# Optimization experiments

Hardware: AMD Instinct MI355X
Metric: run time of the kernel (lower is better)

## Reference

```python
import jax, jax.numpy as jnp
import numpy as np

D = 2048  # input_dimensions (== seq_len, required by the module's math)
H = 8192  # hidden_dimensions
B = 4
S = D


def setup_inputs() -> dict:
    key = jax.random.key(0)
    ks = jax.random.split(key, 13)
    scale_in = 1.0 / np.sqrt(D)
    scale_hid = 1.0 / np.sqrt(H)
    def lin(k, fan_in, fan_out, s):
        return jax.random.normal(k, (fan_in, fan_out), jnp.float32) * s
    inp = {"x": jax.random.normal(ks[0], (B, S, D), jnp.float32)}
    names = ["q", "k", "v"]
    for i, n in enumerate(names):
        inp[f"{n}_w1"] = lin(ks[1 + 4 * i], D, H, scale_in)
        inp[f"{n}_b1"] = jnp.zeros((H,), jnp.float32)
        inp[f"{n}_w2"] = lin(ks[2 + 4 * i], H, D, scale_hid)
        inp[f"{n}_b2"] = jnp.zeros((D,), jnp.float32)
    return inp


def _mlp(x, w1, b1, w2, b2):
    # Linear(D,H) -> ReLU -> Linear(H,D)
    h = jax.nn.relu(jnp.einsum("bsd,dh->bsh", x, w1) + b1)
    return jnp.einsum("bsh,hd->bsd", h, w2) + b2


def reference(x, q_w1, q_b1, q_w2, q_b2, k_w1, k_b1, k_w2, k_b2,
              v_w1, v_b1, v_w2, v_b2):
    Q = _mlp(x, q_w1, q_b1, q_w2, q_b2)
    K = _mlp(x, k_w1, k_b1, k_w2, k_b2)
    V = _mlp(x, v_w1, v_b1, v_w2, v_b2)
    # scores: Q @ K^T  -> [B, S, S]  (no 1/sqrt(d) scaling in original)
    scores = jnp.einsum("bsd,btd->bst", Q, K)
    # nn.Softmax(dim=1): over axis 1 (rows), NOT the usual last axis
    probs = jax.nn.softmax(scores, axis=1)
    # original computes V @ probs (requires S == D)
    out = jnp.einsum("bsd,bdt->bst", V, probs)
    return out
```

## Files before the change

### kernel.cpp

```cpp
#include <hip/hip_runtime.h>
#include <cstdint>
#include <cstddef>

typedef __attribute__((ext_vector_type(8))) short short8;
typedef __attribute__((ext_vector_type(4))) short short4v;
typedef __attribute__((ext_vector_type(4))) float f32x4;
typedef __attribute__((ext_vector_type(4))) int i32x4;

#define DEV __device__ __forceinline__

constexpr int DD = 2048;
constexpr int HHID = 8192;
constexpr int BB = 4;
constexpr int SS = 2048;
constexpr size_t NX = (size_t)BB * SS * DD;
constexpr size_t NW = (size_t)DD * HHID;
constexpr size_t NH = (size_t)BB * SS * HHID;

constexpr size_t OFF_XH  = 0;
constexpr size_t OFF_XA1 = OFF_XH + NX * 2;
constexpr size_t OFF_XA2 = OFF_XA1 + NX;
constexpr size_t OFF_WA1 = OFF_XA2 + NX;
constexpr size_t OFF_WA2 = OFF_WA1 + NW;
constexpr size_t OFF_WHV = OFF_WA1;
constexpr size_t OFF_HH  = OFF_WA2 + NW;
constexpr size_t OFF_HL  = OFF_HH + NH * 2;
constexpr size_t OFF_QKH = OFF_HL + NH * 2;
constexpr size_t OFF_QKL = OFF_QKH + NX * 2;
constexpr size_t OFF_QA1 = OFF_QKL + NX * 2;
constexpr size_t OFF_QA2 = OFF_QA1 + NX;
constexpr size_t OFF_KA1 = OFF_QA2 + NX;
constexpr size_t OFF_KA2 = OFF_KA1 + NX;
constexpr size_t OFF_HA1 = OFF_KA2 + NX;
constexpr size_t OFF_HA2 = OFF_HA1 + NH;
constexpr size_t OFF_V   = OFF_HA2 + NH;
constexpr size_t OFF_XS  = OFF_V + NX * 2;
constexpr size_t OFF_HS  = OFF_XS + 32768;
constexpr size_t OFF_QS  = OFF_HS + 32768;
constexpr size_t OFF_KS  = OFF_QS + 32768;
constexpr size_t OFF_CM  = OFF_KS + 32768;
constexpr size_t WS_TOTAL = OFF_CM + 32768;
constexpr size_t OFF_ST = OFF_HH;
constexpr size_t OFF_PT = OFF_HL;

__device__ __align__(256) unsigned char g_ws[WS_TOTAL];

DEV unsigned char* wsbase(unsigned char* p) { return p ? p : (unsigned char*)g_ws; }
DEV short f2bf(float v) { __bf16 b = (__bf16)v; return __builtin_bit_cast(short, b); }
DEV float bf2f(short s) { return (float)__builtin_bit_cast(__bf16, s); }

template <typename T> DEV void nts(T v, T* p) { __builtin_nontemporal_store(v, p); }
template <typename T> DEV T ntl(const T* p) { return __builtin_nontemporal_load(p); }

DEV void gl16(const short* g, short* l) {
  __builtin_amdgcn_global_load_lds((const __attribute__((address_space(1))) void*)g,
                                   (__attribute__((address_space(3))) void*)l, 16, 0, 0);
}
DEV void gl16b(const signed char* g, signed char* l) {
  __builtin_amdgcn_global_load_lds((const __attribute__((address_space(1))) void*)g,
                                   (__attribute__((address_space(3))) void*)l, 16, 0, 0);
}

DEV void raster2d(int rem, int gx, int grp, int& by, int& bx) {
  const int tpg = grp * gx;
  const int gidx = rem / tpg;
  const int o = rem - gidx * tpg;
  const int r = o / grp;
  by = gidx * grp + (o - r * grp);
  bx = r;
}

__global__ void cast_hi_k(const float* __restrict__ x, unsigned char* wsb,
                          size_t oh, size_t n4) {
  unsigned char* ws = wsbase(wsb);
  short4v* OH = (short4v*)(ws + oh);
  const f32x4* X = (const f32x4*)x;
  for (size_t i = (size_t)blockIdx.x * blockDim.x + threadIdx.x; i < n4;
       i += (size_t)gridDim.x * blockDim.x) {
    const f32x4 v = ntl(&X[i]);
    short4v hs;
#pragma unroll
    for (int e = 0; e < 4; ++e) hs[e] = f2bf(v[e]);
    OH[i] = hs;
  }
}

__launch_bounds__(256)
__global__ void quant_x_k(const float* __restrict__ x, unsigned char* wsb,
                          size_t oa1, size_t oa2, size_t oxs) {
  unsigned char* ws = wsbase(wsb);
  signed char* A1 = (signed char*)(ws + oa1);
  signed char* A2 = (signed char*)(ws + oa2);
  float* XS = (float*)(ws + oxs);
  const int row = blockIdx.x;
  const float* xr = x + (size_t)row * 2048;
  const int tid = threadIdx.x, lane = tid & 63;
  const f32x4 v0 = *(const f32x4*)&xr[tid * 8];
  const f32x4 v1 = *(const f32x4*)&xr[tid * 8 + 4];
  float m = 0.0f;
#pragma unroll
  for (int e = 0; e < 4; ++e) m = fmaxf(m, fmaxf(fabsf(v0[e]), fabsf(v1[e])));
#pragma unroll
  for (int o = 32; o; o >>= 1) m = fmaxf(m, __shfl_xor(m, o));
  __shared__ float rb[4];
  if (lane == 0) rb[tid >> 6] = m;
  __syncthreads();
  m = fmaxf(fmaxf(rb[0], rb[1]), fmaxf(rb[2], rb[3]));
  const float inv = (m > 1e-30f) ? 127.0f / m : 0.0f;
  if (tid == 0) XS[row] = m * (1.0f / 127.0f);
  unsigned int w1a = 0, w1b = 0, w2a = 0, w2b = 0;
#pragma unroll
  for (int e = 0; e < 8; ++e) {
    const float xv = (e < 4) ? v0[e] : v1[e - 4];
    const float q = xv * inv;
    const float a1f = rintf(q);
    int ia2 = (int)rintf((q - a1f) * 256.0f);
    ia2 = ia2 > 127 ? 127 : (ia2 < -127 ? -127 : ia2);
    const unsigned int b1 = (unsigned char)(signed char)(int)a1f;
    const unsigned int b2 = (unsigned char)(signed char)ia2;
    if (e < 4) { w1a |= b1 << (8 * e); w2a |= b2 << (8 * e); }
    else       { w1b |= b1 << (8 * (e - 4)); w2b |= b2 << (8 * (e - 4)); }
  }
  const size_t o = (size_t)row * 2048 + tid * 8;
  *(unsigned int*)&A1[o] = w1a; *(unsigned int*)&A1[o + 4] = w1b;
  *(unsigned int*)&A2[o] = w2a; *(unsigned int*)&A2[o + 4] = w2b;
}

__launch_bounds__(1024)
__global__ void rowquant_k(unsigned char* wsb, size_t hho, size_t hlo,
                           size_t oa1, size_t oa2, size_t oso, int rowlen) {
  unsigned char* ws = wsbase(wsb);
  const int row = blockIdx.x, tid = threadIdx.x, lane = tid & 63, wv = tid >> 6;
  const int nw = blockDim.x >> 6;
  const short8 hi = ntl((const short8*)((const short*)(ws + hho) + (size_t)row * rowlen) + tid);
  const short8 lo = ntl((const short8*)((const short*)(ws + hlo) + (size_t)row * rowlen) + tid);
  float v[8]; float m = 0.0f;
#pragma unroll
  for (int e = 0; e < 8; ++e) {
    v[e] = bf2f(hi[e]) + bf2f(lo[e]);
    m = fmaxf(m, fabsf(v[e]));
  }
#pragma unroll
  for (int o = 32; o; o >>= 1) m = fmaxf(m, __shfl_xor(m, o));
  __shared__ float rb[16];
  if (lane == 0) rb[wv] = m;
  __syncthreads();
  m = rb[0];
  for (int i = 1; i < nw; ++i) m = fmaxf(m, rb[i]);
  const float inv = (m > 1e-30f) ? 127.0f / m : 0.0f;
  if (tid == 0) ((float*)(ws + oso))[row] = m * (1.0f / 127.0f);
  unsigned int w1a = 0, w1b = 0, w2a = 0, w2b = 0;
#pragma unroll
  for (int e = 0; e < 8; ++e) {
    const float q = v[e] * inv;
    const float a1f = rintf(q);
    int ia2 = (int)rintf((q - a1f) * 256.0f);
    ia2 = ia2 > 127 ? 127 : (ia2 < -127 ? -127 : ia2);
    const unsigned int b1 = (unsigned char)(signed char)(int)a1f;
    const unsigned int b2 = (unsigned char)(signed char)ia2;
    if (e < 4) { w1a |= b1 << (8 * e); w2a |= b2 << (8 * e); }
    else       { w1b |= b1 << (8 * (e - 4)); w2b |= b2 << (8 * (e - 4)); }
  }
  const size_t o = (size_t)row * rowlen + tid * 8;
  signed char* A1 = (signed char*)(ws + oa1);
  signed char* A2 = (signed char*)(ws + oa2);
  *(unsigned int*)&A1[o] = w1a; *(unsigned int*)&A1[o + 4] = w1b;
  *(unsigned int*)&A2[o] = w2a; *(unsigned int*)&A2[o + 4] = w2b;
}

__launch_bounds__(256)
__global__ void colmax_k(const float* __restrict__ w, unsigned char* wsb,
                         size_t omax, int R, int C) {
  unsigned char* ws = wsbase(wsb);
  unsigned int* MX = (unsigned int*)(ws + omax);
  const int col = blockIdx.x * 256 + threadIdx.x;
  const int r0 = blockIdx.y * 128;
  float m = 0.0f;
  for (int r = 0; r < 128; ++r) m = fmaxf(m, fabsf(w[(size_t)(r0 + r) * C + col]));
  atomicMax(&MX[col], __float_as_uint(m));
}

__global__ void scalefix_k(unsigned char* wsb, size_t off, int n) {
  unsigned char* ws = wsbase(wsb);
  const int i = blockIdx.x * 256 + threadIdx.x;
  if (i < n) {
    float* p = (float*)(ws + off);
    const unsigned int u = ((const unsigned int*)p)[i];
    p[i] = __uint_as_float(u) * (1.0f / 127.0f);
  }
}

__global__ void transpose_quant_k(const float* __restrict__ src, unsigned char* wsb,
                                  size_t oa1, size_t oa2, size_t osc, int R, int C) {
  __shared__ float t[32][33];
  unsigned char* ws = wsbase(wsb);
  signed char* A1 = (signed char*)(ws + oa1);
  signed char* A2 = (signed char*)(ws + oa2);
  const float* SC = (const float*)(ws + osc);
  const int c0 = blockIdx.x << 5, r0 = blockIdx.y << 5;
  const int x = threadIdx.x, y = threadIdx.y;
#pragma unroll
  for (int i = 0; i < 4; ++i) {
    const int rr = y + (i << 3);
    t[rr][x] = ntl(&src[(size_t)(r0 + rr) * C + c0 + x]);
  }
  __syncthreads();
#pragma unroll
  for (int i = 0; i < 4; ++i) {
    const int oc = y + (i << 3);
    const float v = t[x][oc];
    const float s = SC[c0 + oc];
    const float inv = (s > 1e-38f) ? 1.0f / s : 0.0f;
    const float q = v * inv;
    const float a1f = rintf(q);
    int ia2 = (int)rintf((q - a1f) * 256.0f);
    ia2 = ia2 > 127 ? 127 : (ia2 < -127 ? -127 : ia2);
    const size_t o = (size_t)(c0 + oc) * R + r0 + x;
    A1[o] = (signed char)(int)a1f;
    A2[o] = (signed char)ia2;
  }
}

__global__ void transpose_cast_k(const float* __restrict__ src, unsigned char* wsb,
                                 size_t oh, int R, int C) {
  __shared__ float t[32][33];
  unsigned char* ws = wsbase(wsb);
  short* OH = (short*)(ws + oh);
  const int c0 = blockIdx.x << 5, r0 = blockIdx.y << 5;
  const int x = threadIdx.x, y = threadIdx.y;
#pragma unroll
  for (int i = 0; i < 4; ++i) {
    const int rr = y + (i << 3);
    t[rr][x] = ntl(&src[(size_t)(r0 + rr) * C + c0 + x]);
  }
  __syncthreads();
#pragma unroll
  for (int i = 0; i < 4; ++i) {
    const int oc = y + (i << 3);
    OH[(size_t)(c0 + oc) * R + r0 + x] = f2bf(t[x][oc]);
  }
}

DEV i32x4 mfma_i8(i32x4 a, i32x4 b, i32x4 c) {
  return __builtin_amdgcn_mfma_i32_16x16x64_i8(a, b, c, 0, 0, 0);
}
DEV i32x4 rfi8(const signed char* base, int lstride, int L, int row, int fg) {
  return *(const i32x4*)&base[L * lstride + row * 64 + ((fg ^ ((row >> 1) & 3)) << 4)];
}

template <bool RELU, int STORE>
__launch_bounds__(512, 2)
__global__ void gemm_i8_k(unsigned char* wsb,
                          size_t a1o, size_t a2o, size_t b1o, size_t b2o,
                          size_t aso, size_t bso, const float* __restrict__ bias,
                          size_t o0, size_t o1, int M, int N, int K,
                          int gx, int gxy, int grp) {
  __shared__ alignas(16) signed char lds8[114688];

  unsigned char* ws = wsbase(wsb);
  const int tid = threadIdx.x;
  const int lane = tid & 63;
  const int wave = tid >> 6;
  const int wm = (wave >> 2) << 6;
  const int wn = (wave & 3) << 6;
  const int fr = lane & 15;
  const int fg = lane >> 4;

  const int nwg = gridDim.x;
  const int q8 = nwg >> 3;
  const int id = (blockIdx.x & 7) * q8 + (blockIdx.x >> 3);
  const int bz = id / gxy;
  const int rem = id - bz * gxy;
  int by, bx;
  raster2d(rem, gx, grp, by, bx);
  const int brow = by << 7;
  const int bcol = bx << 8;

  const size_t batchA = (size_t)bz * M * K;
  const size_t batchB = (STORE == 2) ? (size_t)bz * N * K : 0;
  const signed char* Xa1 = (const signed char*)(ws + a1o) + batchA;
  const signed char* Xa2 = (const signed char*)(ws + a2o) + batchA;
  const signed char* Wa1 = (const signed char*)(ws + b1o) + batchB;
  const signed char* Wa2 = (const signed char*)(ws + b2o) + batchB;
  const float* AS = (const float*)(ws + aso) + (size_t)bz * M;
  const float* BS = (const float*)(ws + bso) + ((STORE == 2) ? (size_t)bz * N : 0);

  const int ar = tid >> 2, ac = tid & 3;
  const size_t aOff = (size_t)(brow + ar) * K + ((ac ^ ((ar >> 1) & 3)) << 4);
  size_t bOff[2];
#pragma unroll
  for (int h = 0; h < 2; ++h) {
    const int G = tid + h * 512;
    const int r = G >> 2, c = G & 3;
    bOff[h] = (size_t)(bcol + r) * K + ((c ^ ((r >> 1) & 3)) << 4);
  }

  auto stageA = [&](int slotBase, int tt) {
    const int ko = tt * 64;
    gl16b(Xa1 + aOff + ko, &lds8[slotBase + (tid << 4)]);
    gl16b(Xa2 + aOff + ko, &lds8[slotBase + 8192 + (tid << 4)]);
  };
  auto stageB = [&](int slotBase, int tt) {
    const int ko = tt * 64;
#pragma unroll
    for (int h = 0; h < 2; ++h) {
      gl16b(Wa1 + bOff[h] + ko, &lds8[slotBase + ((tid + h * 512) << 4)]);
      gl16b(Wa2 + bOff[h] + ko, &lds8[slotBase + 16384 + ((tid + h * 512) << 4)]);
    }
  };

  const int nt = K / 64;
  i32x4 I1[4][4] = {};
  i32x4 I2[4][4] = {};

  stageA(0, 0);
  stageB(49152, 0);
  if (nt > 1) { stageA(16384, 1); stageB(49152 + 32768, 1); }
  if (nt > 1) { asm volatile("s_waitcnt vmcnt(6)" ::: "memory"); }
  else        { asm volatile("s_waitcnt vmcnt(0)" ::: "memory"); }
  __builtin_amdgcn_s_barrier();

  for (int t = 0; t < nt; ++t) {
    const signed char* aS = &lds8[(t % 3) * 16384];
    const signed char* bS = &lds8[49152 + (t & 1) * 32768];
    const int sA2 = ((t + 2) % 3) * 16384;
    const int sB2 = 49152 + (t & 1) * 32768;
    const bool pf = (t + 2 < nt);
    i32x4 bf[4][2], af[2][2];

    if (pf) stageA(sA2, t + 2);
#pragma unroll
    for (int j = 0; j < 4; ++j) {
      bf[j][0] = rfi8(bS, 16384, 0, wn + j * 16 + fr, fg);
      bf[j][1] = rfi8(bS, 16384, 1, wn + j * 16 + fr, fg);
    }
#pragma unroll
    for (int i = 0; i < 2; ++i) {
      af[i][0] = rfi8(aS, 8192, 0, wm + i * 16 + fr, fg);
      af[i][1] = rfi8(aS, 8192, 1, wm + i * 16 + fr, fg);
    }
    __builtin_amdgcn_s_setprio(1);
#pragma unroll
    for (int i = 0; i < 2; ++i)
#pragma unroll
      for (int j = 0; j < 4; ++j) {
        I1[i][j] = mfma_i8(af[i][0], bf[j][0], I1[i][j]);
        I2[i][j] = mfma_i8(af[i][0], bf[j][1], I2[i][j]);
        I2[i][j] = mfma_i8(af[i][1], bf[j][0], I2[i][j]);
      }
    __builtin_amdgcn_s_setprio(0);
    __builtin_amdgcn_s_barrier();

    asm volatile("" ::: "memory");
    if (pf) stageB(sB2, t + 2);
#pragma unroll
    for (int i = 0; i < 2; ++i) {
      af[i][0] = rfi8(aS, 8192, 0, wm + (2 + i) * 16 + fr, fg);
      af[i][1] = rfi8(aS, 8192, 1, wm + (2 + i) * 16 + fr, fg);
    }
    __builtin_amdgcn_s_setprio(1);
#pragma unroll
    for (int i = 0; i < 2; ++i)
#pragma unroll
      for (int j = 0; j < 4; ++j) {
        I1[2 + i][j] = mfma_i8(af[i][0], bf[j][0], I1[2 + i][j]);
        I2[2 + i][j] = mfma_i8(af[i][0], bf[j][1], I2[2 + i][j]);
        I2[2 + i][j] = mfma_i8(af[i][1], bf[j][0], I2[2 + i][j]);
      }
    __builtin_amdgcn_s_setprio(0);
    if (pf) { asm volatile("s_waitcnt vmcnt(6)" ::: "memory"); }
    else    { asm volatile("s_waitcnt vmcnt(0)" ::: "memory"); }
    __builtin_amdgcn_s_barrier();
  }

  const int fq4 = fg << 2;
  if constexpr (STORE == 0) {
    short* ldsS = (short*)lds8;
    short* Oh = (short*)(ws + o0);
    short* Ol = (short*)(ws + o1);
#pragma unroll
    for (int rd = 0; rd < 2; ++rd) {
      __builtin_amdgcn_s_barrier();
#pragma unroll
      for (int i = 0; i < 4; ++i) {
        const int rl = wm + i * 16 + fq4;
        const f32x4 sa4 = *(const f32x4*)&AS[brow + rl];
#pragma unroll
        for (int j = 0; j < 4; ++j) {
          const int cl = wn + j * 16 + fr;
          const float sb = BS[bcol + cl];
          const float bv = bias ? bias[bcol + cl] : 0.0f;
#pragma unroll
          for (int e = 0; e < 4; ++e) {
            float u = ((float)I1[i][j][e] + (float)I2[i][j][e] * (1.0f / 256.0f)) *
                          (sa4[e] * sb) + bv;
            if (RELU) u = fmaxf(u, 0.0f);
            short v;
            if (rd == 0) {
              v = f2bf(u);
            } else {
              const short hb = f2bf(u);
              v = f2bf(u - bf2f(hb));
            }
            ldsS[(rl + e) * 264 + cl] = v;
          }
        }
      }
      __builtin_amdgcn_s_barrier();
      short* gout = (rd == 0) ? Oh : Ol;
#pragma unroll
      for (int gi = 0; gi < 8; ++gi) {
        const int g = gi * 512 + tid;
        const int row = g >> 5, cg = g & 31;
        const short8 v = *(const short8*)&ldsS[row * 264 + cg * 8];
        nts(v, (short8*)&gout[(size_t)(brow + row) * N + bcol + cg * 8]);
      }
    }
  } else {
    float* Of = (float*)(ws + o0) + (size_t)bz * M * N;
    float* ldsf = (float*)lds8;
#pragma unroll
    for (int h2 = 0; h2 < 2; ++h2) {
      __builtin_amdgcn_s_barrier();
      if ((wn >> 7) == h2) {
#pragma unroll
        for (int i = 0; i < 4; ++i) {
          const int rl = wm + i * 16 + fq4;
          const f32x4 sa4 = *(const f32x4*)&AS[brow + rl];
#pragma unroll
          for (int j = 0; j < 4; ++j) {
            const int cp = (wn & 127) + j * 16 + fr;
            const float sb = BS[bcol + wn + j * 16 + fr];
            f32x4 u;
#pragma unroll
            for (int e = 0; e < 4; ++e)
              u[e] = ((float)I1[i][j][e] + (float)I2[i][j][e] * (1.0f / 256.0f)) *
                     (sa4[e] * sb);
            *(f32x4*)&ldsf[cp * 132 + rl] = u;
          }
        }
      }
      __builtin_amdgcn_s_barrier();
#pragma unroll
      for (int gi = 0; gi < 8; ++gi) {
        const int g = gi * 512 + tid;
        const int tr = g >> 5, tc4 = (g & 31) << 2;
        const f32x4 v = *(const f32x4*)&ldsf[tr * 132 + tc4];
        nts(v, (f32x4*)&Of[(size_t)(bcol + h2 * 128 + tr) * M + brow + tc4]);
      }
    }
  }
}

constexpr int CH = 8192;

DEV short8 read_frag1(const short* base, int row, int s, int fg) {
  return *(const short8*)&base[row * 64 + ((((s << 2) | fg) ^ (row & 7)) << 3)];
}

DEV f32x4 mfma16(short8 a, short8 b, f32x4 c) {
  return __builtin_amdgcn_mfma_f32_16x16x32_bf16(a, b, c, 0, 0, 0);
}

template <bool RELU, int STORE>
__launch_bounds__(512, 2)
__global__ void gemm8_k(unsigned char* wsb,
                        size_t aoff0, size_t boff0,
                        const float* __restrict__ bias,
                        size_t ooff0, float* __restrict__ optr,
                        int M, int N, int K, int gx, int gxy, int grp) {
  __shared__ alignas(16) short lds[10 * CH];

  unsigned char* ws = wsbase(wsb);
  const int tid = threadIdx.x;
  const int lane = tid & 63;
  const int wave = tid >> 6;
  const int wm = (wave >> 2) << 7;
  const int wn = (wave & 3) << 6;

  const int nwg = gridDim.x;
  const int q8 = nwg >> 3;
  const int id = (blockIdx.x & 7) * q8 + (blockIdx.x >> 3);
  const int bz = id / gxy;
  const int rem = id - bz * gxy;
  int by, bx;
  raster2d(rem, gx, grp, by, bx);
  const int brow = by << 8;
  const int bcol = bx << 8;

  const short* A0 = (const short*)(ws + aoff0) + (size_t)bz * M * K;
  const short* B0g = (const short*)(ws + boff0) + (size_t)bz * N * K;

  size_t aSrc[2][2], bSrc[2][2];
#pragma unroll
  for (int h = 0; h < 2; ++h) {
    const int G = tid + h * 512;
    const int r = G >> 3, c = G & 7;
#pragma unroll
    for (int qq = 0; qq < 2; ++qq) {
      aSrc[qq][h] = (size_t)(brow + qq * 128 + r) * K + (size_t)((c ^ (r & 7)) << 3);
      bSrc[qq][h] = (size_t)(bcol + qq * 128 + r) * K + (size_t)((c ^ (r & 7)) << 3);
    }
  }
  const int ldst0 = tid << 3;

  auto issueA = [&](int slot, int qq, int tt) {
    short* dst = &lds[slot + qq * CH];
    const size_t ka = (size_t)tt * 64;
    gl16(A0 + aSrc[qq][0] + ka, dst + ldst0);
    gl16(A0 + aSrc[qq][1] + ka, dst + ldst0 + CH / 2);
  };
  auto issueB = [&](int slot, int qq, int tt) {
    short* dst = &lds[slot + qq * CH];
    const size_t ka = (size_t)tt * 64;
    gl16(B0g + bSrc[qq][0] + ka, dst + ldst0);
    gl16(B0g + bSrc[qq][1] + ka, dst + ldst0 + CH / 2);
  };

  const int nt = K / 64;
  const int fr = lane & 15;
  const int fg = lane >> 4;

  f32x4 acc[8][4] = {};

  issueA(0, 0, 0); issueA(0, 1, 0);
  issueB(6 * CH, 0, 0); issueB(6 * CH, 1, 0);
  if (nt > 1) {
    issueA(2 * CH, 0, 1); issueA(2 * CH, 1, 1);
    issueB(8 * CH, 0, 1); issueB(8 * CH, 1, 1);
    asm volatile("s_waitcnt vmcnt(8)" ::: "memory");
  } else {
    asm volatile("s_waitcnt vmcnt(0)" ::: "memory");
  }
  __builtin_amdgcn_s_barrier();

  for (int t = 0; t < nt; ++t) {
    const short* aBase = &lds[(t % 3) * (2 * CH)];
    const short* bBase = &lds[6 * CH + (t & 1) * (2 * CH)];
    const int sA2 = ((t + 2) % 3) * (2 * CH);
    const int sB  = 6 * CH + (t & 1) * (2 * CH);
    const bool pf = (t + 2 < nt);
    short8 bfr[4][2], av[4][2];

    if (pf) { issueA(sA2, 0, t + 2); issueA(sA2, 1, t + 2); }
#pragma unroll
    for (int j = 0; j < 4; ++j) {
      bfr[j][0] = read_frag1(bBase, wn + j * 16 + fr, 0, fg);
      bfr[j][1] = read_frag1(bBase, wn + j * 16 + fr, 1, fg);
    }
#pragma unroll
    for (int i = 0; i < 4; ++i) {
      av[i][0] = read_frag1(aBase, wm + i * 16 + fr, 0, fg);
      av[i][1] = read_frag1(aBase, wm + i * 16 + fr, 1, fg);
    }
    __builtin_amdgcn_s_setprio(1);
#pragma unroll
    for (int i = 0; i < 4; ++i)
#pragma unroll
      for (int j = 0; j < 4; ++j) {
        acc[i][j] = mfma16(av[i][0], bfr[j][0], acc[i][j]);
        acc[i][j] = mfma16(av[i][1], bfr[j][1], acc[i][j]);
      }
    __builtin_amdgcn_s_setprio(0);
    __builtin_amdgcn_s_barrier();

    asm volatile("" ::: "memory");
    if (pf) { issueB(sB, 0, t + 2); issueB(sB, 1, t + 2); }
#pragma unroll
    for (int i = 0; i < 4; ++i) {
      av[i][0] = read_frag1(aBase, wm + 64 + i * 16 + fr, 0, fg);
      av[i][1] = read_frag1(aBase, wm + 64 + i * 16 + fr, 1, fg);
    }
    __builtin_amdgcn_s_setprio(1);
#pragma unroll
    for (int i = 0; i < 4; ++i)
#pragma unroll
      for (int j = 0; j < 4; ++j) {
        acc[4 + i][j] = mfma16(av[i][0], bfr[j][0], acc[4 + i][j]);
        acc[4 + i][j] = mfma16(av[i][1], bfr[j][1], acc[4 + i][j]);
      }
    __builtin_amdgcn_s_setprio(0);
    if (pf) {
      asm volatile("s_waitcnt vmcnt(8)" ::: "memory");
    } else {
      asm volatile("s_waitcnt vmcnt(0)" ::: "memory");
    }
    __builtin_amdgcn_s_barrier();
  }

  const int fq4 = (lane >> 4) << 2;
  if constexpr (STORE == 1) {
    short* Oh = (short*)(ws + ooff0);
    __builtin_amdgcn_s_barrier();
#pragma unroll
    for (int i = 0; i < 8; ++i) {
      const int rl = wm + i * 16 + fq4;
#pragma unroll
      for (int j = 0; j < 4; ++j) {
        const int cl = wn + j * 16 + fr;
        const float bv = bias ? bias[bcol + cl] : 0.0f;
#pragma unroll
        for (int e = 0; e < 4; ++e) {
          float u = acc[i][j][e] + bv;
          if (RELU) u = fmaxf(u, 0.0f);
          lds[(rl + e) * 264 + cl] = f2bf(u);
        }
      }
    }
    __builtin_amdgcn_s_barrier();
#pragma unroll
    for (int gi = 0; gi < 16; ++gi) {
      const int g = gi * 512 + tid;
      const int row = g >> 5, cg = g & 31;
      const short8 v = *(const short8*)&lds[row * 264 + cg * 8];
      nts(v, (short8*)&Oh[(size_t)(brow + row) * N + bcol + cg * 8]);
    }
  } else {
    float* Op = optr + (size_t)bz * M * N;
    float* ldsf = (float*)lds;
#pragma unroll
    for (int h = 0; h < 2; ++h) {
      __builtin_amdgcn_s_barrier();
      if ((wm & 128) == (h << 7)) {
#pragma unroll
        for (int i = 0; i < 8; ++i) {
          const int rp = (wm & 127) + i * 16 + fq4;
#pragma unroll
          for (int j = 0; j < 4; ++j) {
            const int cl = wn + j * 16 + fr;
#pragma unroll
            for (int e = 0; e < 4; ++e)
              ldsf[(rp + e) * 258 + cl] = acc[i][j][e];
          }
        }
      }
      __builtin_amdgcn_s_barrier();
#pragma unroll
      for (int gi = 0; gi < 16; ++gi) {
        const int g = gi * 512 + tid;
        const int tr = g >> 6, tc4 = (g & 63) << 2;
        const f32x4 v = *(const f32x4*)&ldsf[tr * 258 + tc4];
        nts(v, (f32x4*)&Op[(size_t)(brow + h * 128 + tr) * N + bcol + tc4]);
      }
    }
  }
}

__launch_bounds__(256)
__global__ void softmax_rows_k(unsigned char* wsb, size_t st, size_t pt) {
  constexpr int S = 2048;
  unsigned char* ws = wsbase(wsb);
  const f32x4* row = (const f32x4*)((const float*)(ws + st) + (size_t)blockIdx.x * S);
  short4v* out = (short4v*)((short*)(ws + pt) + (size_t)blockIdx.x * S);
  const int tid = threadIdx.x, lane = tid & 63, wv = tid >> 6;
  const f32x4 a = ntl(&row[tid]);
  const f32x4 b = ntl(&row[tid + 256]);
  float m = fmaxf(fmaxf(fmaxf(a[0], a[1]), fmaxf(a[2], a[3])),
                  fmaxf(fmaxf(b[0], b[1]), fmaxf(b[2], b[3])));
#pragma unroll
  for (int o = 32; o; o >>= 1) m = fmaxf(m, __shfl_xor(m, o));
  __shared__ float rb[8];
  if (lane == 0) rb[wv] = m;
  __syncthreads();
  m = fmaxf(fmaxf(rb[0], rb[1]), fmaxf(rb[2], rb[3]));
  float e[8];
  float s = 0.0f;
#pragma unroll
  for (int q = 0; q < 4; ++q) { e[q] = expf(a[q] - m); s += e[q]; }
#pragma unroll
  for (int q = 0; q < 4; ++q) { e[4 + q] = expf(b[q] - m); s += e[4 + q]; }
#pragma unroll
  for (int o = 32; o; o >>= 1) s += __shfl_xor(s, o);
  if (lane == 0) rb[4 + wv] = s;
  __syncthreads();
  s = rb[4] + rb[5] + rb[6] + rb[7];
  const float inv = 1.0f / s;
  short4v o1, o2;
#pragma unroll
  for (int q = 0; q < 4; ++q) { o1[q] = f2bf(e[q] * inv); o2[q] = f2bf(e[4 + q] * inv); }
  nts(o1, &out[tid]);
  nts(o2, &out[tid + 256]);
}

extern "C" void kernel_launch(void* const* d_in, const int* in_sizes, int n_in,
                              void* d_out, int out_size, void* d_ws, size_t ws_size,
                              hipStream_t stream) {
  const float* x   = (const float*)d_in[0];
  const float* qw1 = (const float*)d_in[1];
  const float* qb1 = (const float*)d_in[2];
  const float* qw2 = (const float*)d_in[3];
  const float* qb2 = (const float*)d_in[4];
  const float* kw1 = (const float*)d_in[5];
  const float* kb1 = (const float*)d_in[6];
  const float* kw2 = (const float*)d_in[7];
  const float* kb2 = (const float*)d_in[8];
  const float* vw1 = (const float*)d_in[9];
  const float* vb1 = (const float*)d_in[10];
  const float* vw2 = (const float*)d_in[11];
  const float* vb2 = (const float*)d_in[12];
  float* out = (float*)d_out;
  unsigned char* wsb = (ws_size >= WS_TOTAL) ? (unsigned char*)d_ws : nullptr;
  unsigned char* wsr;
  if (wsb) wsr = wsb;
  else { hipError_t e = hipGetSymbolAddress((void**)&wsr, HIP_SYMBOL(g_ws)); (void)e; }

  const int M = BB * SS;
  dim3 blk(512);
  dim3 tb(32, 8);

  quant_x_k<<<8192, 256, 0, stream>>>(x, wsb, OFF_XA1, OFF_XA2, OFF_XS);
  cast_hi_k<<<4096, 256, 0, stream>>>(x, wsb, OFF_XH, NX / 4);

  hipMemsetAsync(wsr + OFF_CM, 0, 32768, stream);
  colmax_k<<<dim3(HHID / 256, DD / 128), 256, 0, stream>>>(qw1, wsb, OFF_CM, DD, HHID);
  scalefix_k<<<32, 256, 0, stream>>>(wsb, OFF_CM, HHID);
  transpose_quant_k<<<dim3(HHID / 32, DD / 32), tb, 0, stream>>>(qw1, wsb, OFF_WA1, OFF_WA2, OFF_CM, DD, HHID);
  gemm_i8_k<true, 0><<<2048, blk, 0, stream>>>(wsb, OFF_XA1, OFF_XA2, OFF_WA1, OFF_WA2,
                                               OFF_XS, OFF_CM, qb1, OFF_HH, OFF_HL,
                                               M, HHID, DD, 32, 2048, 8);
  rowquant_k<<<8192, 1024, 0, stream>>>(wsb, OFF_HH, OFF_HL, OFF_HA1, OFF_HA2, OFF_HS, HHID);
  hipMemsetAsync(wsr + OFF_CM, 0, 32768, stream);
  colmax_k<<<dim3(DD / 256, HHID / 128), 256, 0, stream>>>(qw2, wsb, OFF_CM, HHID, DD);
  scalefix_k<<<8, 256, 0, stream>>>(wsb, OFF_CM, DD);
  transpose_quant_k<<<dim3(DD / 32, HHID / 32), tb, 0, stream>>>(qw2, wsb, OFF_WA1, OFF_WA2, OFF_CM, HHID, DD);
  gemm_i8_k<false, 0><<<512, blk, 0, stream>>>(wsb, OFF_HA1, OFF_HA2, OFF_WA1, OFF_WA2,
                                               OFF_HS, OFF_CM, qb2, OFF_QKH, OFF_QKL,
                                               M, DD, HHID, 8, 512, 8);
  rowquant_k<<<8192, 256, 0, stream>>>(wsb, OFF_QKH, OFF_QKL, OFF_QA1, OFF_QA2, OFF_QS, DD);

  hipMemsetAsync(wsr + OFF_CM, 0, 32768, stream);
  colmax_k<<<dim3(HHID / 256, DD / 128), 256, 0, stream>>>(kw1, wsb, OFF_CM, DD, HHID);
  scalefix_k<<<32, 256, 0, stream>>>(wsb, OFF_CM, HHID);
  transpose_quant_k<<<dim3(HHID / 32, DD / 32), tb, 0, stream>>>(kw1, wsb, OFF_WA1, OFF_WA2, OFF_CM, DD, HHID);
  gemm_i8_k<true, 0><<<2048, blk, 0, stream>>>(wsb, OFF_XA1, OFF_XA2, OFF_WA1, OFF_WA2,
                                               OFF_XS, OFF_CM, kb1, OFF_HH, OFF_HL,
                                               M, HHID, DD, 32, 2048, 8);
  rowquant_k<<<8192, 1024, 0, stream>>>(wsb, OFF_HH, OFF_HL, OFF_HA1, OFF_HA2, OFF_HS, HHID);
  hipMemsetAsync(wsr + OFF_CM, 0, 32768, stream);
  colmax_k<<<dim3(DD / 256, HHID / 128), 256, 0, stream>>>(kw2, wsb, OFF_CM, HHID, DD);
  scalefix_k<<<8, 256, 0, stream>>>(wsb, OFF_CM, DD);
  transpose_quant_k<<<dim3(DD / 32, HHID / 32), tb, 0, stream>>>(kw2, wsb, OFF_WA1, OFF_WA2, OFF_CM, HHID, DD);
  gemm_i8_k<false, 0><<<512, blk, 0, stream>>>(wsb, OFF_HA1, OFF_HA2, OFF_WA1, OFF_WA2,
                                               OFF_HS, OFF_CM, kb2, OFF_QKH, OFF_QKL,
                                               M, DD, HHID, 8, 512, 8);
  rowquant_k<<<8192, 256, 0, stream>>>(wsb, OFF_QKH, OFF_QKL, OFF_KA1, OFF_KA2, OFF_KS, DD);

  transpose_cast_k<<<dim3(HHID / 32, DD / 32), tb, 0, stream>>>(vw1, wsb, OFF_WHV, DD, HHID);
  gemm8_k<true, 1><<<1024, blk, 0, stream>>>(
      wsb, OFF_XH, OFF_WHV, vb1, OFF_HH, nullptr, M, HHID, DD, 32, 1024, 4);
  transpose_cast_k<<<dim3(DD / 32, HHID / 32), tb, 0, stream>>>(vw2, wsb, OFF_WHV, HHID, DD);
  gemm8_k<false, 1><<<256, blk, 0, stream>>>(
      wsb, OFF_HH, OFF_WHV, vb2, OFF_V, nullptr, M, DD, HHID, 8, 256, 4);

  gemm_i8_k<false, 2><<<512, blk, 0, stream>>>(wsb, OFF_QA1, OFF_QA2, OFF_KA1, OFF_KA2,
                                               OFF_QS, OFF_KS, nullptr, OFF_ST, 0,
                                               SS, SS, DD, 8, 128, 8);

  softmax_rows_k<<<BB * SS, 256, 0, stream>>>(wsb, OFF_ST, OFF_PT);

  gemm8_k<false, 3><<<256, blk, 0, stream>>>(
      wsb, OFF_V, OFF_PT, nullptr, 0, out, SS, SS, DD, 8, 64, 4);
}
```

Before: 2.672 ms.

## Move V MLP and final PV product from bf16 GEMMs to split-int8 GEMMs

Replaces the bf16 MFMA path for the V projection MLP and the final V@P product with the two-part int8 GEMM path already used for Q and K. This adds per-column weight quantization for the V weights, and a softmax kernel that writes quantized int8 probabilities with a per-row scale. It also adds an fp32 output mode to the int8 GEMM. The aim is to use the higher int8 MFMA throughput and smaller operands, at the cost of extra quantization passes and some precision risk.

```diff
diff --git a/kernel.cpp b/kernel.cpp
--- a/kernel.cpp
+++ b/kernel.cpp
@@ -17,12 +17,10 @@
 constexpr size_t NW = (size_t)DD * HHID;
 constexpr size_t NH = (size_t)BB * SS * HHID;
 
-constexpr size_t OFF_XH  = 0;
-constexpr size_t OFF_XA1 = OFF_XH + NX * 2;
+constexpr size_t OFF_XA1 = 0;
 constexpr size_t OFF_XA2 = OFF_XA1 + NX;
 constexpr size_t OFF_WA1 = OFF_XA2 + NX;
 constexpr size_t OFF_WA2 = OFF_WA1 + NW;
-constexpr size_t OFF_WHV = OFF_WA1;
 constexpr size_t OFF_HH  = OFF_WA2 + NW;
 constexpr size_t OFF_HL  = OFF_HH + NH * 2;
 constexpr size_t OFF_QKH = OFF_HL + NH * 2;
@@ -33,15 +31,21 @@
 constexpr size_t OFF_KA2 = OFF_KA1 + NX;
 constexpr size_t OFF_HA1 = OFF_KA2 + NX;
 constexpr size_t OFF_HA2 = OFF_HA1 + NH;
-constexpr size_t OFF_V   = OFF_HA2 + NH;
-constexpr size_t OFF_XS  = OFF_V + NX * 2;
+constexpr size_t OFF_XS  = OFF_HA2 + NH;
 constexpr size_t OFF_HS  = OFF_XS + 32768;
 constexpr size_t OFF_QS  = OFF_HS + 32768;
 constexpr size_t OFF_KS  = OFF_QS + 32768;
-constexpr size_t OFF_CM  = OFF_KS + 32768;
+constexpr size_t OFF_VS  = OFF_KS + 32768;
+constexpr size_t OFF_PS  = OFF_VS + 32768;
+constexpr size_t OFF_CM  = OFF_PS + 32768;
 constexpr size_t WS_TOTAL = OFF_CM + 32768;
-constexpr size_t OFF_ST = OFF_HH;
-constexpr size_t OFF_PT = OFF_HL;
+constexpr size_t OFF_ST  = OFF_HH;
+constexpr size_t OFF_PA1 = OFF_HL;
+constexpr size_t OFF_PA2 = OFF_HL + NX;
+constexpr size_t OFF_VH  = OFF_QKH;
+constexpr size_t OFF_VL  = OFF_QKL;
+constexpr size_t OFF_VA1 = OFF_XA1;
+constexpr size_t OFF_VA2 = OFF_XA2;
 
 __device__ __align__(256) unsigned char g_ws[WS_TOTAL];
 
@@ -52,10 +56,6 @@
 template <typename T> DEV void nts(T v, T* p) { __builtin_nontemporal_store(v, p); }
 template <typename T> DEV T ntl(const T* p) { return __builtin_nontemporal_load(p); }
 
-DEV void gl16(const short* g, short* l) {
-  __builtin_amdgcn_global_load_lds((const __attribute__((address_space(1))) void*)g,
-                                   (__attribute__((address_space(3))) void*)l, 16, 0, 0);
-}
 DEV void gl16b(const signed char* g, signed char* l) {
   __builtin_amdgcn_global_load_lds((const __attribute__((address_space(1))) void*)g,
                                    (__attribute__((address_space(3))) void*)l, 16, 0, 0);
@@ -68,21 +68,6 @@
   const int r = o / grp;
   by = gidx * grp + (o - r * grp);
   bx = r;
-}
-
-__global__ void cast_hi_k(const float* __restrict__ x, unsigned char* wsb,
-                          size_t oh, size_t n4) {
-  unsigned char* ws = wsbase(wsb);
-  short4v* OH = (short4v*)(ws + oh);
-  const f32x4* X = (const f32x4*)x;
-  for (size_t i = (size_t)blockIdx.x * blockDim.x + threadIdx.x; i < n4;
-       i += (size_t)gridDim.x * blockDim.x) {
-    const f32x4 v = ntl(&X[i]);
-    short4v hs;
-#pragma unroll
-    for (int e = 0; e < 4; ++e) hs[e] = f2bf(v[e]);
-    OH[i] = hs;
-  }
 }
 
 __launch_bounds__(256)
@@ -221,26 +206,6 @@
   }
 }
 
-__global__ void transpose_cast_k(const float* __restrict__ src, unsigned char* wsb,
-                                 size_t oh, int R, int C) {
-  __shared__ float t[32][33];
-  unsigned char* ws = wsbase(wsb);
-  short* OH = (short*)(ws + oh);
-  const int c0 = blockIdx.x << 5, r0 = blockIdx.y << 5;
-  const int x = threadIdx.x, y = threadIdx.y;
-#pragma unroll
-  for (int i = 0; i < 4; ++i) {
-    const int rr = y + (i << 3);
-    t[rr][x] = ntl(&src[(size_t)(r0 + rr) * C + c0 + x]);
-  }
-  __syncthreads();
-#pragma unroll
-  for (int i = 0; i < 4; ++i) {
-    const int oc = y + (i << 3);
-    OH[(size_t)(c0 + oc) * R + r0 + x] = f2bf(t[x][oc]);
-  }
-}
-
 DEV i32x4 mfma_i8(i32x4 a, i32x4 b, i32x4 c) {
   return __builtin_amdgcn_mfma_i32_16x16x64_i8(a, b, c, 0, 0, 0);
 }
@@ -254,7 +219,7 @@
                           size_t a1o, size_t a2o, size_t b1o, size_t b2o,
                           size_t aso, size_t bso, const float* __restrict__ bias,
                           size_t o0, size_t o1, int M, int N, int K,
-                          int gx, int gxy, int grp) {
+                          int gx, int gxy, int grp, float* __restrict__ optr) {
   __shared__ alignas(16) signed char lds8[114688];
 
   unsigned char* ws = wsbase(wsb);
@@ -277,13 +242,13 @@
   const int bcol = bx << 8;
 
   const size_t batchA = (size_t)bz * M * K;
-  const size_t batchB = (STORE == 2) ? (size_t)bz * N * K : 0;
+  const size_t batchB = (STORE >= 2) ? (size_t)bz * N * K : 0;
   const signed char* Xa1 = (const signed char*)(ws + a1o) + batchA;
   const signed char* Xa2 = (const signed char*)(ws + a2o) + batchA;
   const signed char* Wa1 = (const signed char*)(ws + b1o) + batchB;
   const signed char* Wa2 = (const signed char*)(ws + b2o) + batchB;
   const float* AS = (const float*)(ws + aso) + (size_t)bz * M;
-  const float* BS = (const float*)(ws + bso) + ((STORE == 2) ? (size_t)bz * N : 0);
+  const float* BS = (const float*)(ws + bso) + ((STORE >= 2) ? (size_t)bz * N : 0);
 
   const int ar = tid >> 2, ac = tid & 3;
   const size_t aOff = (size_t)(brow + ar) * K + ((ac ^ ((ar >> 1) & 3)) << 4);
@@ -416,7 +381,7 @@
         nts(v, (short8*)&gout[(size_t)(brow + row) * N + bcol + cg * 8]);
       }
     }
-  } else {
+  } else if constexpr (STORE == 2) {
     float* Of = (float*)(ws + o0) + (size_t)bz * M * N;
     float* ldsf = (float*)lds8;
 #pragma unroll
@@ -449,209 +414,48 @@
         nts(v, (f32x4*)&Of[(size_t)(bcol + h2 * 128 + tr) * M + brow + tc4]);
       }
     }
-  }
-}
-
-constexpr int CH = 8192;
-
-DEV short8 read_frag1(const short* base, int row, int s, int fg) {
-  return *(const short8*)&base[row * 64 + ((((s << 2) | fg) ^ (row & 7)) << 3)];
-}
-
-DEV f32x4 mfma16(short8 a, short8 b, f32x4 c) {
-  return __builtin_amdgcn_mfma_f32_16x16x32_bf16(a, b, c, 0, 0, 0);
-}
-
-template <bool RELU, int STORE>
-__launch_bounds__(512, 2)
-__global__ void gemm8_k(unsigned char* wsb,
-                        size_t aoff0, size_t boff0,
-                        const float* __restrict__ bias,
-                        size_t ooff0, float* __restrict__ optr,
-                        int M, int N, int K, int gx, int gxy, int grp) {
-  __shared__ alignas(16) short lds[10 * CH];
-
-  unsigned char* ws = wsbase(wsb);
-  const int tid = threadIdx.x;
-  const int lane = tid & 63;
-  const int wave = tid >> 6;
-  const int wm = (wave >> 2) << 7;
-  const int wn = (wave & 3) << 6;
-
-  const int nwg = gridDim.x;
-  const int q8 = nwg >> 3;
-  const int id = (blockIdx.x & 7) * q8 + (blockIdx.x >> 3);
-  const int bz = id / gxy;
-  const int rem = id - bz * gxy;
-  int by, bx;
-  raster2d(rem, gx, grp, by, bx);
-  const int brow = by << 8;
-  const int bcol = bx << 8;
-
-  const short* A0 = (const short*)(ws + aoff0) + (size_t)bz * M * K;
-  const short* B0g = (const short*)(ws + boff0) + (size_t)bz * N * K;
-
-  size_t aSrc[2][2], bSrc[2][2];
-#pragma unroll
-  for (int h = 0; h < 2; ++h) {
-    const int G = tid + h * 512;
-    const int r = G >> 3, c = G & 7;
-#pragma unroll
-    for (int qq = 0; qq < 2; ++qq) {
-      aSrc[qq][h] = (size_t)(brow + qq * 128 + r) * K + (size_t)((c ^ (r & 7)) << 3);
-      bSrc[qq][h] = (size_t)(bcol + qq * 128 + r) * K + (size_t)((c ^ (r & 7)) << 3);
-    }
-  }
-  const int ldst0 = tid << 3;
-
-  auto issueA = [&](int slot, int qq, int tt) {
-    short* dst = &lds[slot + qq * CH];
-    const size_t ka = (size_t)tt * 64;
-    gl16(A0 + aSrc[qq][0] + ka, dst + ldst0);
-    gl16(A0 + aSrc[qq][1] + ka, dst + ldst0 + CH / 2);
-  };
-  auto issueB = [&](int slot, int qq, int tt) {
-    short* dst = &lds[slot + qq * CH];
-    const size_t ka = (size_t)tt * 64;
-    gl16(B0g + bSrc[qq][0] + ka, dst + ldst0);
-    gl16(B0g + bSrc[qq][1] + ka, dst + ldst0 + CH / 2);
-  };
-
-  const int nt = K / 64;
-  const int fr = lane & 15;
-  const int fg = lane >> 4;
-
-  f32x4 acc[8][4] = {};
-
-  issueA(0, 0, 0); issueA(0, 1, 0);
-  issueB(6 * CH, 0, 0); issueB(6 * CH, 1, 0);
-  if (nt > 1) {
-    issueA(2 * CH, 0, 1); issueA(2 * CH, 1, 1);
-    issueB(8 * CH, 0, 1); issueB(8 * CH, 1, 1);
-    asm volatile("s_waitcnt vmcnt(8)" ::: "memory");
-  } else {
-    asm volatile("s_waitcnt vmcnt(0)" ::: "memory");
-  }
-  __builtin_amdgcn_s_barrier();
-
-  for (int t = 0; t < nt; ++t) {
-    const short* aBase = &lds[(t % 3) * (2 * CH)];
-    const short* bBase = &lds[6 * CH + (t & 1) * (2 * CH)];
-    const int sA2 = ((t + 2) % 3) * (2 * CH);
-    const int sB  = 6 * CH + (t & 1) * (2 * CH);
-    const bool pf = (t + 2 < nt);
-    short8 bfr[4][2], av[4][2];
-
-    if (pf) { issueA(sA2, 0, t + 2); issueA(sA2, 1, t + 2); }
-#pragma unroll
-    for (int j = 0; j < 4; ++j) {
-      bfr[j][0] = read_frag1(bBase, wn + j * 16 + fr, 0, fg);
-      bfr[j][1] = read_frag1(bBase, wn + j * 16 + fr, 1, fg);
-    }
-#pragma unroll
-    for (int i = 0; i < 4; ++i) {
-      av[i][0] = read_frag1(aBase, wm + i * 16 + fr, 0, fg);
-      av[i][1] = read_frag1(aBase, wm + i * 16 + fr, 1, fg);
-    }
-    __builtin_amdgcn_s_setprio(1);
-#pragma unroll
-    for (int i = 0; i < 4; ++i)
-#pragma unroll
-      for (int j = 0; j < 4; ++j) {
-        acc[i][j] = mfma16(av[i][0], bfr[j][0], acc[i][j]);
-        acc[i][j] = mfma16(av[i][1], bfr[j][1], acc[i][j]);
-      }
-    __builtin_amdgcn_s_setprio(0);
-    __builtin_amdgcn_s_barrier();
-
-    asm volatile("" ::: "memory");
-    if (pf) { issueB(sB, 0, t + 2); issueB(sB, 1, t + 2); }
-#pragma unroll
-    for (int i = 0; i < 4; ++i) {
-      av[i][0] = read_frag1(aBase, wm + 64 + i * 16 + fr, 0, fg);
-      av[i][1] = read_frag1(aBase, wm + 64 + i * 16 + fr, 1, fg);
-    }
-    __builtin_amdgcn_s_setprio(1);
-#pragma unroll
-    for (int i = 0; i < 4; ++i)
-#pragma unroll
-      for (int j = 0; j < 4; ++j) {
-        acc[4 + i][j] = mfma16(av[i][0], bfr[j][0], acc[4 + i][j]);
-        acc[4 + i][j] = mfma16(av[i][1], bfr[j][1], acc[4 + i][j]);
-      }
-    __builtin_amdgcn_s_setprio(0);
-    if (pf) {
-      asm volatile("s_waitcnt vmcnt(8)" ::: "memory");
-    } else {
-      asm volatile("s_waitcnt vmcnt(0)" ::: "memory");
-    }
-    __builtin_amdgcn_s_barrier();
-  }
-
-  const int fq4 = (lane >> 4) << 2;
-  if constexpr (STORE == 1) {
-    short* Oh = (short*)(ws + ooff0);
-    __builtin_amdgcn_s_barrier();
-#pragma unroll
-    for (int i = 0; i < 8; ++i) {
-      const int rl = wm + i * 16 + fq4;
-#pragma unroll
-      for (int j = 0; j < 4; ++j) {
-        const int cl = wn + j * 16 + fr;
-        const float bv = bias ? bias[bcol + cl] : 0.0f;
-#pragma unroll
-        for (int e = 0; e < 4; ++e) {
-          float u = acc[i][j][e] + bv;
-          if (RELU) u = fmaxf(u, 0.0f);
-          lds[(rl + e) * 264 + cl] = f2bf(u);
-        }
-      }
-    }
-    __builtin_amdgcn_s_barrier();
-#pragma unroll
-    for (int gi = 0; gi < 16; ++gi) {
-      const int g = gi * 512 + tid;
-      const int row = g >> 5, cg = g & 31;
-      const short8 v = *(const short8*)&lds[row * 264 + cg * 8];
-      nts(v, (short8*)&Oh[(size_t)(brow + row) * N + bcol + cg * 8]);
-    }
   } else {
     float* Op = optr + (size_t)bz * M * N;
-    float* ldsf = (float*)lds;
-#pragma unroll
-    for (int h = 0; h < 2; ++h) {
+    float* ldsf = (float*)lds8;
+#pragma unroll
+    for (int h2 = 0; h2 < 2; ++h2) {
       __builtin_amdgcn_s_barrier();
-      if ((wm & 128) == (h << 7)) {
-#pragma unroll
-        for (int i = 0; i < 8; ++i) {
-          const int rp = (wm & 127) + i * 16 + fq4;
+      if ((wm >> 6) == h2) {
+#pragma unroll
+        for (int i = 0; i < 4; ++i) {
+          const int grow = wm + i * 16 + fq4;
+          const int rl = grow & 63;
+          const f32x4 sa4 = *(const f32x4*)&AS[brow + grow];
 #pragma unroll
           for (int j = 0; j < 4; ++j) {
             const int cl = wn + j * 16 + fr;
+            const float sb = BS[bcol + cl];
 #pragma unroll
             for (int e = 0; e < 4; ++e)
-              ldsf[(rp + e) * 258 + cl] = acc[i][j][e];
+              ldsf[(rl + e) * 264 + cl] =
+                  ((float)I1[i][j][e] + (float)I2[i][j][e] * (1.0f / 256.0f)) *
+                  (sa4[e] * sb);
           }
         }
       }
       __builtin_amdgcn_s_barrier();
 #pragma unroll
-      for (int gi = 0; gi < 16; ++gi) {
+      for (int gi = 0; gi < 8; ++gi) {
         const int g = gi * 512 + tid;
         const int tr = g >> 6, tc4 = (g & 63) << 2;
-        const f32x4 v = *(const f32x4*)&ldsf[tr * 258 + tc4];
-        nts(v, (f32x4*)&Op[(size_t)(brow + h * 128 + tr) * N + bcol + tc4]);
+        const f32x4 v = *(const f32x4*)&ldsf[tr * 264 + tc4];
+        nts(v, (f32x4*)&Op[(size_t)(brow + h2 * 64 + tr) * N + bcol + tc4]);
       }
     }
   }
 }
 
 __launch_bounds__(256)
-__global__ void softmax_rows_k(unsigned char* wsb, size_t st, size_t pt) {
+__global__ void softmax_quant_k(unsigned char* wsb, size_t st,
+                                size_t pa1, size_t pa2, size_t ps) {
   constexpr int S = 2048;
   unsigned char* ws = wsbase(wsb);
   const f32x4* row = (const f32x4*)((const float*)(ws + st) + (size_t)blockIdx.x * S);
-  short4v* out = (short4v*)((short*)(ws + pt) + (size_t)blockIdx.x * S);
   const int tid = threadIdx.x, lane = tid & 63, wv = tid >> 6;
   const f32x4 a = ntl(&row[tid]);
   const f32x4 b = ntl(&row[tid + 256]);
@@ -675,11 +479,26 @@
   __syncthreads();
   s = rb[4] + rb[5] + rb[6] + rb[7];
   const float inv = 1.0f / s;
-  short4v o1, o2;
-#pragma unroll
-  for (int q = 0; q < 4; ++q) { o1[q] = f2bf(e[q] * inv); o2[q] = f2bf(e[4 + q] * inv); }
-  nts(o1, &out[tid]);
-  nts(o2, &out[tid + 256]);
+  if (tid == 0) ((float*)(ws + ps))[blockIdx.x] = inv * (1.0f / 127.0f);
+  unsigned int w1a = 0, w1b = 0, w2a = 0, w2b = 0;
+#pragma unroll
+  for (int q = 0; q < 8; ++q) {
+    const float qv = 127.0f * e[q];
+    const float a1f = rintf(qv);
+    int ia2 = (int)rintf((qv - a1f) * 256.0f);
+    ia2 = ia2 > 127 ? 127 : (ia2 < -127 ? -127 : ia2);
+    const unsigned int b1 = (unsigned char)(signed char)(int)a1f;
+    const unsigned int b2 = (unsigned char)(signed char)ia2;
+    if (q < 4) { w1a |= b1 << (8 * q); w2a |= b2 << (8 * q); }
+    else       { w1b |= b1 << (8 * (q - 4)); w2b |= b2 << (8 * (q - 4)); }
+  }
+  signed char* A1 = (signed char*)(ws + pa1);
+  signed char* A2 = (signed char*)(ws + pa2);
+  const size_t ro = (size_t)blockIdx.x * S;
+  nts(w1a, (unsigned int*)&A1[ro + tid * 4]);
+  nts(w1b, (unsigned int*)&A1[ro + 1024 + tid * 4]);
+  nts(w2a, (unsigned int*)&A2[ro + tid * 4]);
+  nts(w2b, (unsigned int*)&A2[ro + 1024 + tid * 4]);
 }
 
 extern "C" void kernel_launch(void* const* d_in, const int* in_sizes, int n_in,
@@ -709,7 +528,6 @@
   dim3 tb(32, 8);
 
   quant_x_k<<<8192, 256, 0, stream>>>(x, wsb, OFF_XA1, OFF_XA2, OFF_XS);
-  cast_hi_k<<<4096, 256, 0, stream>>>(x, wsb, OFF_XH, NX / 4);
 
   hipMemsetAsync(wsr + OFF_CM, 0, 32768, stream);
   colmax_k<<<dim3(HHID / 256, DD / 128), 256, 0, stream>>>(qw1, wsb, OFF_CM, DD, HHID);
@@ -717,7 +535,7 @@
   transpose_quant_k<<<dim3(HHID / 32, DD / 32), tb, 0, stream>>>(qw1, wsb, OFF_WA1, OFF_WA2, OFF_CM, DD, HHID);
   gemm_i8_k<true, 0><<<2048, blk, 0, stream>>>(wsb, OFF_XA1, OFF_XA2, OFF_WA1, OFF_WA2,
                                                OFF_XS, OFF_CM, qb1, OFF_HH, OFF_HL,
-                                               M, HHID, DD, 32, 2048, 8);
+                                               M, HHID, DD, 32, 2048, 8, nullptr);
   rowquant_k<<<8192, 1024, 0, stream>>>(wsb, OFF_HH, OFF_HL, OFF_HA1, OFF_HA2, OFF_HS, HHID);
   hipMemsetAsync(wsr + OFF_CM, 0, 32768, stream);
   colmax_k<<<dim3(DD / 256, HHID / 128), 256, 0, stream>>>(qw2, wsb, OFF_CM, HHID, DD);
@@ -725,7 +543,7 @@
   transpose_quant_k<<<dim3(DD / 32, HHID / 32), tb, 0, stream>>>(qw2, wsb, OFF_WA1, OFF_WA2, OFF_CM, HHID, DD);
   gemm_i8_k<false, 0><<<512, blk, 0, stream>>>(wsb, OFF_HA1, OFF_HA2, OFF_WA1, OFF_WA2,
                                                OFF_HS, OFF_CM, qb2, OFF_QKH, OFF_QKL,
-                                               M, DD, HHID, 8, 512, 8);
+                                               M, DD, HHID, 8, 512, 8, nullptr);
   rowquant_k<<<8192, 256, 0, stream>>>(wsb, OFF_QKH, OFF_QKL, OFF_QA1, OFF_QA2, OFF_QS, DD);
 
   hipMemsetAsync(wsr + OFF_CM, 0, 32768, stream);
@@ -734,7 +552,7 @@
   transpose_quant_k<<<dim3(HHID / 32, DD / 32), tb, 0, stream>>>(kw1, wsb, OFF_WA1, OFF_WA2, OFF_CM, DD, HHID);
   gemm_i8_k<true, 0><<<2048, blk, 0, stream>>>(wsb, OFF_XA1, OFF_XA2, OFF_WA1, OFF_WA2,
                                                OFF_XS, OFF_CM, kb1, OFF_HH, OFF_HL,
-                                               M, HHID, DD, 32, 2048, 8);
+                                               M, HHID, DD, 32, 2048, 8, nullptr);
   rowquant_k<<<8192, 1024, 0, stream>>>(wsb, OFF_HH, OFF_HL, OFF_HA1, OFF_HA2, OFF_HS, HHID);
   hipMemsetAsync(wsr + OFF_CM, 0, 32768, stream);
   colmax_k<<<dim3(DD / 256, HHID / 128), 256, 0, stream>>>(kw2, wsb, OFF_CM, HHID, DD);
@@ -742,22 +560,33 @@
   transpose_quant_k<<<dim3(DD / 32, HHID / 32), tb, 0, stream>>>(kw2, wsb, OFF_WA1, OFF_WA2, OFF_CM, HHID, DD);
   gemm_i8_k<false, 0><<<512, blk, 0, stream>>>(wsb, OFF_HA1, OFF_HA2, OFF_WA1, OFF_WA2,
                                                OFF_HS, OFF_CM, kb2, OFF_QKH, OFF_QKL,
-                                               M, DD, HHID, 8, 512, 8);
+                                               M, DD, HHID, 8, 512, 8, nullptr);
   rowquant_k<<<8192, 256, 0, stream>>>(wsb, OFF_QKH, OFF_QKL, OFF_KA1, OFF_KA2, OFF_KS, DD);
 
-  transpose_cast_k<<<dim3(HHID / 32, DD / 32), tb, 0, stream>>>(vw1, wsb, OFF_WHV, DD, HHID);
-  gemm8_k<true, 1><<<1024, blk, 0, stream>>>(
-      wsb, OFF_XH, OFF_WHV, vb1, OFF_HH, nullptr, M, HHID, DD, 32, 1024, 4);
-  transpose_cast_k<<<dim3(DD / 32, HHID / 32), tb, 0, stream>>>(vw2, wsb, OFF_WHV, HHID, DD);
-  gemm8_k<false, 1><<<256, blk, 0, stream>>>(
-      wsb, OFF_HH, OFF_WHV, vb2, OFF_V, nullptr, M, DD, HHID, 8, 256, 4);
+  hipMemsetAsync(wsr + OFF_CM, 0, 32768, stream);
+  colmax_k<<<dim3(HHID / 256, DD / 128), 256, 0, stream>>>(vw1, wsb, OFF_CM, DD, HHID);
+  scalefix_k<<<32, 256, 0, stream>>>(wsb, OFF_CM, HHID);
+  transpose_quant_k<<<dim3(HHID / 32, DD / 32), tb, 0, stream>>>(vw1, wsb, OFF_WA1, OFF_WA2, OFF_CM, DD, HHID);
+  gemm_i8_k<true, 0><<<2048, blk, 0, stream>>>(wsb, OFF_XA1, OFF_XA2, OFF_WA1, OFF_WA2,
+                                               OFF_XS, OFF_CM, vb1, OFF_HH, OFF_HL,
+                                               M, HHID, DD, 32, 2048, 8, nullptr);
+  rowquant_k<<<8192, 1024, 0, stream>>>(wsb, OFF_HH, OFF_HL, OFF_HA1, OFF_HA2, OFF_HS, HHID);
+  hipMemsetAsync(wsr + OFF_CM, 0, 32768, stream);
+  colmax_k<<<dim3(DD / 256, HHID / 128), 256, 0, stream>>>(vw2, wsb, OFF_CM, HHID, DD);
+  scalefix_k<<<8, 256, 0, stream>>>(wsb, OFF_CM, DD);
+  transpose_quant_k<<<dim3(DD / 32, HHID / 32), tb, 0, stream>>>(vw2, wsb, OFF_WA1, OFF_WA2, OFF_CM, HHID, DD);
+  gemm_i8_k<false, 0><<<512, blk, 0, stream>>>(wsb, OFF_HA1, OFF_HA2, OFF_WA1, OFF_WA2,
+                                               OFF_HS, OFF_CM, vb2, OFF_VH, OFF_VL,
+                                               M, DD, HHID, 8, 512, 8, nullptr);
+  rowquant_k<<<8192, 256, 0, stream>>>(wsb, OFF_VH, OFF_VL, OFF_VA1, OFF_VA2, OFF_VS, DD);
 
   gemm_i8_k<false, 2><<<512, blk, 0, stream>>>(wsb, OFF_QA1, OFF_QA2, OFF_KA1, OFF_KA2,
                                                OFF_QS, OFF_KS, nullptr, OFF_ST, 0,
-                                               SS, SS, DD, 8, 128, 8);
-
-  softmax_rows_k<<<BB * SS, 256, 0, stream>>>(wsb, OFF_ST, OFF_PT);
-
-  gemm8_k<false, 3><<<256, blk, 0, stream>>>(
-      wsb, OFF_V, OFF_PT, nullptr, 0, out, SS, SS, DD, 8, 64, 4);
-}
+                                               SS, SS, DD, 8, 128, 8, nullptr);
+
+  softmax_quant_k<<<BB * SS, 256, 0, stream>>>(wsb, OFF_ST, OFF_PA1, OFF_PA2, OFF_PS);
+
+  gemm_i8_k<false, 3><<<512, blk, 0, stream>>>(wsb, OFF_VA1, OFF_VA2, OFF_PA1, OFF_PA2,
+                                               OFF_VS, OFF_PS, nullptr, 0, 0,
+                                               SS, SS, DD, 8, 128, 8, out);
+}
```

Result: slower. 3.175 ms (+18.8%).
